# Performance work log

Hardware: AMD Instinct MI355X
Metric: run time of the kernel (lower is better)

Reference implementation:

```python
import jax, jax.numpy as jnp
import numpy as np

B, N = 4, 2048
EXPR, TIME, POSF = 512, 128, 128
H, HD = 8, 64
D = EXPR  # total_features_out_dim == d_model == 512
TOTAL_IN = EXPR + TIME + POSF  # 768
EPS_RMS = 1e-6


def _lin(key, fan_in, fan_out):
    kw, kb = jax.random.split(key)
    lim = 1.0 / np.sqrt(fan_in)
    W = jax.random.uniform(kw, (fan_in, fan_out), minval=-lim, maxval=lim, dtype=jnp.float32)
    b = jax.random.uniform(kb, (fan_out,), minval=-lim, maxval=lim, dtype=jnp.float32)
    return W, b


def setup_inputs() -> dict:
    key = jax.random.key(0)
    ks = jax.random.split(key, 20)
    inp = {}
    inp["expression_features"] = jax.random.normal(ks[0], (B, N, EXPR), dtype=jnp.float32)
    inp["diffusion_time"] = jax.random.normal(ks[1], (B, TIME), dtype=jnp.float32)
    inp["position_features"] = jax.random.normal(ks[2], (B, N, 3), dtype=jnp.float32)
    # position MLP: 4 -> 64 -> POSF
    inp["pos_w1"], inp["pos_b1"] = _lin(ks[3], 4, 64)
    inp["pos_w2"], inp["pos_b2"] = _lin(ks[4], 64, POSF)
    # expression MLP: EXPR -> 64 -> EXPR
    inp["expr_w1"], inp["expr_b1"] = _lin(ks[5], EXPR, 64)
    inp["expr_w2"], inp["expr_b2"] = _lin(ks[6], 64, EXPR)
    # time transform
    inp["yy_w"], inp["yy_b"] = _lin(ks[7], TIME, TIME)
    # concatenated features linear: TOTAL_IN -> D
    inp["cat_w"], inp["cat_b"] = _lin(ks[8], TOTAL_IN, D)
    # attention projections (headwise gating: q_proj outputs D + H)
    inp["q_w"], inp["q_b"] = _lin(ks[9], D, D + H)
    inp["k_w"], inp["k_b"] = _lin(ks[10], D, D)
    inp["v_w"], inp["v_b"] = _lin(ks[11], D, D)
    inp["o_w"], inp["o_b"] = _lin(ks[12], D, D)
    inp["qn_w"] = jnp.ones((HD,), dtype=jnp.float32)
    inp["kn_w"] = jnp.ones((HD,), dtype=jnp.float32)
    # output heads
    inp["hp_w"], inp["hp_b"] = _lin(ks[13], D, 3)
    inp["he_w"], inp["he_b"] = _lin(ks[14], D, EXPR)
    return inp


def _rmsnorm(x, w):
    xf = x.astype(jnp.float32)
    var = jnp.mean(xf * xf, axis=-1, keepdims=True)
    return (w * (xf * jax.lax.rsqrt(var + EPS_RMS))).astype(x.dtype)


def reference(expression_features, diffusion_time, position_features,
              pos_w1, pos_b1, pos_w2, pos_b2,
              expr_w1, expr_b1, expr_w2, expr_b2,
              yy_w, yy_b, cat_w, cat_b,
              q_w, q_b, k_w, k_b, v_w, v_b, o_w, o_b,
              qn_w, kn_w, hp_w, hp_b, he_w, he_b):
    b, n, _ = expression_features.shape
    # expression MLP
    te = jax.nn.relu(expression_features @ expr_w1 + expr_b1) @ expr_w2 + expr_b2
    # position features: direction + norm -> MLP
    nrm = jnp.linalg.norm(position_features, axis=-1, keepdims=True)
    direction = position_features / (nrm + 1e-7)
    pfeat = jnp.concatenate([direction, nrm], axis=-1)  # (B,N,4)
    tp = jax.nn.relu(pfeat @ pos_w1 + pos_b1) @ pos_w2 + pos_b2
    # diffusion time transform (not last layer)
    tdt = diffusion_time @ yy_w + yy_b  # (B,TIME)
    time_exp = jnp.broadcast_to(tdt[:, None, :], (b, n, tdt.shape[-1]))
    cat = jnp.concatenate([te, time_exp, tp], axis=-1)  # (B,N,TOTAL_IN)
    h = cat @ cat_w + cat_b  # (B,N,D)
    # gated multi-head attention
    qfull = h @ q_w + q_b  # (B,N,D+H)
    Q, gate = qfull[..., :D], qfull[..., D:]  # (B,N,D), (B,N,H)
    K = h @ k_w + k_b
    V = h @ v_w + v_b
    Q = Q.reshape(b, n, H, HD).transpose(0, 2, 1, 3)  # (B,H,N,hd)
    K = K.reshape(b, n, H, HD).transpose(0, 2, 1, 3)
    V = V.reshape(b, n, H, HD).transpose(0, 2, 1, 3)
    Q = _rmsnorm(Q, qn_w)
    K = _rmsnorm(K, kn_w)
    scores = jnp.einsum('bhqd,bhkd->bhqk', Q, K) / np.sqrt(HD)
    attn = jax.nn.softmax(scores.astype(jnp.float32), axis=-1).astype(Q.dtype)
    ao = jnp.einsum('bhqk,bhkd->bhqd', attn, V)  # (B,H,N,hd)
    ao = ao.transpose(0, 2, 1, 3)  # (B,N,H,hd)
    ao = ao * jax.nn.sigmoid(gate)[..., None]  # headwise gating
    ao = ao.reshape(b, n, D)
    out = ao @ o_w + o_b  # (B,N,D)
    expr_out = out @ he_w + he_b  # (B,N,EXPR)
    pos_out = out @ hp_w + hp_b   # (B,N,3)
    return expr_out, pos_out, tdt
```

## Files before the change

kernel.cpp:

```cpp
#include <hip/hip_runtime.h>
#include <math.h>

#define SEQ   2048
#define NROWS 8192

typedef unsigned short ushort_t;
typedef __attribute__((ext_vector_type(8))) short bf16x8;
typedef __attribute__((ext_vector_type(4))) float f32x4;

#define U_EXPR   0ull
#define U_A192   4194304ull
#define U_H      5767168ull
#define U_QKV    9961472ull
#define U_KN     26804224ull
#define U_VT     30998528ull
#define U_AO     35192832ull
#define U_W1T    39387136ull
#define U_W2RAW  39419904ull
#define U_CATWT  39452672ull
#define U_QKVWT  39845888ull
#define U_HEWT   40898560ull
#define U_WPRIME 41160704ull
#define U_WOHE   41259008ull
#define U_F32    41521152ull
#define U_ORAW   41537536ull

#define F_TDT    0
#define F_QKVB   512
#define F_BIASH  2056
#define F_BIASEO 4104
#define F_BIASPO 4616
#define F_WHP    4620

#define DOUT_EXPR 0ull
#define DOUT_POS  4194304ull
#define DOUT_TDT  4218880ull

#define LOG2E 1.44269504088896340736f

static __device__ __forceinline__ ushort_t f2bf(float f) {
    union { float f; unsigned int u; } v; v.f = f;
    unsigned int r = (v.u + 0x7fffu + ((v.u >> 16) & 1u)) >> 16;
    return (ushort_t)r;
}
static __device__ __forceinline__ float bf2f(ushort_t u) {
    union { unsigned int u; float f; } v; v.u = ((unsigned int)u) << 16;
    return v.f;
}

static __device__ __forceinline__ void gload16(const void* g, void* l) {
    __builtin_amdgcn_global_load_lds(
        (const __attribute__((address_space(1))) void*)g,
        (__attribute__((address_space(3))) void*)l,
        16, 0, 0);
}

template <int RELU, int OUT_BF16, int HASBIAS, int BBSTRIDE, int KC>
static __device__ void hgemm_body(
    const ushort_t* __restrict__ A, int lda,
    const ushort_t* __restrict__ Wt, int ldw,
    const float* __restrict__ bias,
    void* __restrict__ Cv, int ldc,
    int N, int bx, int by,
    ushort_t* AsB, ushort_t* BsB)
{
    const int tid = threadIdx.x;
    const int lane = tid & 63, w = tid >> 6;
    const int lo = lane & 15, hi = lane >> 4;
    const int wm = w >> 2, wn = w & 3;
    const long m0 = (long)by * 128;
    const int n0 = bx * 128;

    f32x4 acc[4][2];
#pragma unroll
    for (int mt = 0; mt < 4; ++mt)
#pragma unroll
        for (int nt = 0; nt < 2; ++nt) acc[mt][nt] = (f32x4)0.f;

    auto stage = [&](int kt, int buf) {
#pragma unroll
        for (int i = 0; i < 2; ++i) {
            int c = w * 128 + i * 64 + lane;
            int r = c >> 3, ch = c & 7;
            int sch = ch ^ (r & 7);
            gload16(&A[(m0 + r) * (long)lda + kt + sch * 8],
                    &AsB[buf * 8192 + (w * 128 + i * 64) * 8]);
            gload16(&Wt[(long)(n0 + r) * ldw + kt + sch * 8],
                    &BsB[buf * 8192 + (w * 128 + i * 64) * 8]);
        }
    };

    stage(0, 0);
    __syncthreads();

#pragma unroll
    for (int step = 0; step < KC / 64; ++step) {
        const int cur = step & 1;
        if ((step + 1) * 64 < KC) stage((step + 1) * 64, cur ^ 1);

#pragma unroll
        for (int ks = 0; ks < 2; ++ks) {
            bf16x8 af[4], bfr[2];
#pragma unroll
            for (int mt = 0; mt < 4; ++mt) {
                int m = wm * 64 + mt * 16 + lo;
                af[mt] = *(const bf16x8*)&AsB[cur * 8192 + m * 64 +
                                              (((ks * 4 + hi) ^ (lo & 7)) * 8)];
            }
#pragma unroll
            for (int nt = 0; nt < 2; ++nt) {
                int n = wn * 32 + nt * 16 + lo;
                bfr[nt] = *(const bf16x8*)&BsB[cur * 8192 + n * 64 +
                                               (((ks * 4 + hi) ^ (lo & 7)) * 8)];
            }
#pragma unroll
            for (int mt = 0; mt < 4; ++mt)
#pragma unroll
                for (int nt = 0; nt < 2; ++nt)
                    acc[mt][nt] = __builtin_amdgcn_mfma_f32_16x16x32_bf16(
                        af[mt], bfr[nt], acc[mt][nt], 0, 0, 0);
        }
        __syncthreads();
    }

#pragma unroll
    for (int mt = 0; mt < 4; ++mt)
#pragma unroll
        for (int nt = 0; nt < 2; ++nt) {
            int col = n0 + wn * 32 + nt * 16 + lo;
            if (col < N) {
                float bv = 0.f;
                if (HASBIAS)
                    bv = BBSTRIDE ? bias[(int)(m0 >> 11) * BBSTRIDE + col] : bias[col];
#pragma unroll
                for (int r = 0; r < 4; ++r) {
                    long row = m0 + wm * 64 + mt * 16 + hi * 4 + r;
                    float v = acc[mt][nt][r] + bv;
                    if (RELU) v = fmaxf(v, 0.f);
                    if (OUT_BF16) ((ushort_t*)Cv)[row * (long)ldc + col] = f2bf(v);
                    else          ((float*)Cv)[row * (long)ldc + col] = v;
                }
            }
        }
}

template <int RELU, int OUT_BF16, int HASBIAS, int BBSTRIDE, int KC>
__global__ __launch_bounds__(512) void hgemm(
    const ushort_t* __restrict__ A, int lda,
    const ushort_t* __restrict__ Wt, int ldw,
    const float* __restrict__ bias,
    void* __restrict__ Cv, int ldc, int N, int gx)
{
    __shared__ __align__(16) ushort_t ls[32768];
    const int nwg = gridDim.x;
    const int bid = blockIdx.x;
    const int cpx = nwg >> 3;
    const int swz = (bid & 7) * cpx + (bid >> 3);
    hgemm_body<RELU, OUT_BF16, HASBIAS, BBSTRIDE, KC>(
        A, lda, Wt, ldw, bias, Cv, ldc, N,
        swz % gx, swz / gx, ls, ls + 16384);
}

struct WtSeg { const float* src; ushort_t* dst; int K, N, tK, tile0, dstStride, mode; };
struct WtTable { WtSeg s[10]; };

__global__ __launch_bounds__(256) void wt_transpose(
    WtTable tab, const float* __restrict__ qb, const float* __restrict__ kb,
    const float* __restrict__ vb, float* __restrict__ bias_dst,
    const float* __restrict__ dt, const float* __restrict__ yyw,
    const float* __restrict__ yyb, float* __restrict__ tdt_ws,
    float* __restrict__ out_tail)
{
    const int bid = blockIdx.x;
    const int tid = threadIdx.x;
    if (bid == 665) {
        for (int t = tid; t < 512; t += 256) {
            int b = t >> 7, o = t & 127;
            float s = yyb[o];
            for (int k = 0; k < 128; ++k)
                s = fmaf(dt[b * 128 + k], yyw[k * 128 + o], s);
            tdt_ws[t] = s;
            out_tail[t] = s;
        }
        return;
    }
    if (bid >= 658) {
        int t = (bid - 658) * 256 + tid;
        if (t < 520) bias_dst[t] = qb[t];
        else if (t < 1032) bias_dst[t] = kb[t - 520];
        else if (t < 1544) bias_dst[t] = vb[t - 1032];
        return;
    }
    int si = 0;
#pragma unroll
    for (int i = 1; i < 10; ++i)
        if (bid >= tab.s[i].tile0) si = i;
    const WtSeg sg = tab.s[si];
    const int local = bid - sg.tile0;

    if (sg.mode == 1) {
        long base = (long)local * 16384;
#pragma unroll
        for (int i = 0; i < 8; ++i) {
            long p = base + i * 2048 + tid * 8;
            float4 a = *(const float4*)&sg.src[p];
            float4 b = *(const float4*)&sg.src[p + 4];
            bf16x8 o;
            o[0] = (short)f2bf(a.x); o[1] = (short)f2bf(a.y);
            o[2] = (short)f2bf(a.z); o[3] = (short)f2bf(a.w);
            o[4] = (short)f2bf(b.x); o[5] = (short)f2bf(b.y);
            o[6] = (short)f2bf(b.z); o[7] = (short)f2bf(b.w);
            *(bf16x8*)&sg.dst[p] = o;
        }
        return;
    }

    __shared__ float t[64][65];
    const int k0 = (local % sg.tK) * 64;
    const int n0 = (local / sg.tK) * 64;
#pragma unroll
    for (int i = 0; i < 16; ++i) {
        int e = tid + i * 256;
        int r = e >> 6, c = e & 63;
        float v = 0.f;
        if (k0 + r < sg.K && n0 + c < sg.N)
            v = sg.src[(long)(k0 + r) * sg.N + n0 + c];
        t[r][c] = v;
    }
    __syncthreads();
#pragma unroll
    for (int i = 0; i < 16; ++i) {
        int e = tid + i * 256;
        int rn = e >> 6, ck = e & 63;
        if (n0 + rn < sg.N && k0 + ck < sg.K)
            sg.dst[(long)(n0 + rn) * sg.dstStride + k0 + ck] = f2bf(t[ck][rn]);
    }
}

__global__ __launch_bounds__(512) void prep2mlp_kernel(
    const ushort_t* __restrict__ catwt, const ushort_t* __restrict__ hewt,
    const ushort_t* __restrict__ w2raw, const ushort_t* __restrict__ o_raw,
    ushort_t* __restrict__ wprime, ushort_t* __restrict__ wohe,
    const float* __restrict__ expr_b2, const float* __restrict__ tdt,
    const float* __restrict__ cat_b, const float* __restrict__ o_b,
    const float* __restrict__ he_b, const float* __restrict__ o_w,
    const float* __restrict__ hp_w, const float* __restrict__ hp_b,
    float* __restrict__ bias_h, float* __restrict__ bias_eo,
    float* __restrict__ whp, float* __restrict__ bias_po,
    const ushort_t* __restrict__ expr_bf, const ushort_t* __restrict__ w1t,
    const float* __restrict__ expr_b1,
    const float* __restrict__ pos,
    const float* __restrict__ w1, const float* __restrict__ b1,
    const float* __restrict__ w2, const float* __restrict__ b2,
    ushort_t* __restrict__ a192)
{
    __shared__ __align__(16) ushort_t ls[32768];
    const int bid = blockIdx.x;
    const int tid = threadIdx.x;

    if (bid < 4) {
        hgemm_body<0, 1, 0, 0, 512>(catwt, 768, w2raw, 512, nullptr, wprime, 192,
                                    64, 0, bid, ls, ls + 16384);
        return;
    }
    if (bid < 20) {
        int local = bid - 4;
        hgemm_body<0, 1, 0, 0, 512>(hewt, 512, o_raw, 512, nullptr, wohe, 512,
                                    512, local & 3, local >> 2, ls, ls + 16384);
        return;
    }
    if (bid < 533) {
        const int wid = (bid - 20) * 8 + (tid >> 6);
        const int lane = tid & 63;
        float s = 0.f;
        if (wid < 2048) {
            int b = wid >> 9, n = wid & 511;
            bf16x8 wv = *(const bf16x8*)&catwt[(long)n * 768 + lane * 8];
            float4 e0 = *(const float4*)&expr_b2[lane * 8];
            float4 e1 = *(const float4*)&expr_b2[lane * 8 + 4];
            s = bf2f((ushort_t)wv[0]) * e0.x + bf2f((ushort_t)wv[1]) * e0.y +
                bf2f((ushort_t)wv[2]) * e0.z + bf2f((ushort_t)wv[3]) * e0.w +
                bf2f((ushort_t)wv[4]) * e1.x + bf2f((ushort_t)wv[5]) * e1.y +
                bf2f((ushort_t)wv[6]) * e1.z + bf2f((ushort_t)wv[7]) * e1.w;
            float2 tt = *(const float2*)&tdt[b * 128 + lane * 2];
            s += bf2f(catwt[(long)n * 768 + 512 + lane * 2]) * tt.x;
            s += bf2f(catwt[(long)n * 768 + 513 + lane * 2]) * tt.y;
#pragma unroll
            for (int o = 32; o >= 1; o >>= 1) s += __shfl_xor(s, o);
            if (lane == 0) bias_h[b * 512 + n] = s + cat_b[n];
        } else if (wid < 2560) {
            int n = wid - 2048;
            bf16x8 wv = *(const bf16x8*)&hewt[(long)n * 512 + lane * 8];
            float4 e0 = *(const float4*)&o_b[lane * 8];
            float4 e1 = *(const float4*)&o_b[lane * 8 + 4];
            s = bf2f((ushort_t)wv[0]) * e0.x + bf2f((ushort_t)wv[1]) * e0.y +
                bf2f((ushort_t)wv[2]) * e0.z + bf2f((ushort_t)wv[3]) * e0.w +
                bf2f((ushort_t)wv[4]) * e1.x + bf2f((ushort_t)wv[5]) * e1.y +
                bf2f((ushort_t)wv[6]) * e1.z + bf2f((ushort_t)wv[7]) * e1.w;
#pragma unroll
            for (int o = 32; o >= 1; o >>= 1) s += __shfl_xor(s, o);
            if (lane == 0) bias_eo[n] = s + he_b[n];
        } else if (wid < 4096) {
            int t = wid - 2560;
            int c = t >> 9, k = t & 511;
#pragma unroll
            for (int i = 0; i < 8; ++i) {
                int j = i * 64 + lane;
                s = fmaf(o_w[(long)k * 512 + j], hp_w[j * 3 + c], s);
            }
#pragma unroll
            for (int o = 32; o >= 1; o >>= 1) s += __shfl_xor(s, o);
            if (lane == 0) whp[k * 3 + c] = s;
        } else if (wid < 4099) {
            int c = wid - 4096;
#pragma unroll
            for (int i = 0; i < 8; ++i) {
                int j = i * 64 + lane;
                s = fmaf(o_b[j], hp_w[j * 3 + c], s);
            }
#pragma unroll
            for (int o = 32; o >= 1; o >>= 1) s += __shfl_xor(s, o);
            if (lane == 0) bias_po[c] = s + hp_b[c];
        }
        return;
    }
    if (bid < 597) {
        hgemm_body<1, 1, 1, 0, 512>(expr_bf, 512, w1t, 512, expr_b1, a192, 192,
                                    64, 0, bid - 533, ls, ls + 16384);
        return;
    }

    float* w1s = (float*)ls;
    float* b1s = w1s + 256;
    float* b2s = b1s + 64;
    float* w2t = b2s + 128;
    if (tid < 256) w1s[tid] = w1[tid];
    if (tid >= 256 && tid < 320) b1s[tid - 256] = b1[tid - 256];
    if (tid >= 320 && tid < 448) b2s[tid - 320] = b2[tid - 320];
    for (int i = tid; i < 8192; i += 512) {
        int k = i >> 7, o = i & 127;
        w2t[o * 72 + k] = w2[i];
    }
    __syncthreads();

    const long r = (long)(bid - 597) * 64 + (tid >> 3);
    const int chunk = tid & 7;
    float px = pos[r * 3 + 0], py = pos[r * 3 + 1], pz = pos[r * 3 + 2];
    float nrm = sqrtf(px * px + py * py + pz * pz);
    float inv = 1.f / (nrm + 1e-7f);
    float pf0 = px * inv, pf1 = py * inv, pf2 = pz * inv, pf3 = nrm;

    float h1[64];
#pragma unroll
    for (int o = 0; o < 64; ++o) {
        float a = b1s[o];
        a = fmaf(pf0, w1s[o], a);
        a = fmaf(pf1, w1s[64 + o], a);
        a = fmaf(pf2, w1s[128 + o], a);
        a = fmaf(pf3, w1s[192 + o], a);
        h1[o] = fmaxf(a, 0.f);
    }
    ushort_t* dst = &a192[r * 192 + 64];
#pragma unroll
    for (int j = 0; j < 16; ++j) {
        int o = chunk + 8 * j;
        float s = b2s[o];
#pragma unroll
        for (int i4 = 0; i4 < 16; ++i4) {
            float4 wv = *(const float4*)&w2t[o * 72 + i4 * 4];
            s = fmaf(h1[i4 * 4 + 0], wv.x, s);
            s = fmaf(h1[i4 * 4 + 1], wv.y, s);
            s = fmaf(h1[i4 * 4 + 2], wv.z, s);
            s = fmaf(h1[i4 * 4 + 3], wv.w, s);
        }
        dst[o] = f2bf(s);
    }
}

__global__ __launch_bounds__(256) void qkvpost_kernel(
    const ushort_t* __restrict__ qkv, const float* __restrict__ knw,
    ushort_t* __restrict__ kn, ushort_t* __restrict__ Vt)
{
    __shared__ ushort_t t[64][72];
    __shared__ float knw_s[64];
    const int bh = blockIdx.x, b = bh >> 3, h = bh & 7;
    const int n0 = blockIdx.y * 64;
    const int tid = threadIdx.x;
    if (tid < 64) knw_s[tid] = knw[tid];
#pragma unroll
    for (int i = 0; i < 2; ++i) {
        int c = tid + i * 256;
        int r = c >> 3, ch = c & 7;
        *(bf16x8*)&t[r][ch * 8] =
            *(const bf16x8*)&qkv[(long)(b * SEQ + n0 + r) * 1544 + 1032 + h * 64 + ch * 8];
    }
    __syncthreads();
#pragma unroll
    for (int i = 0; i < 2; ++i) {
        int c = tid + i * 256;
        int r = c >> 3, ch = c & 7;
        bf16x8 kv = *(const bf16x8*)&qkv[(long)(b * SEQ + n0 + r) * 1544 + 520 + h * 64 + ch * 8];
        float x[8], ss = 0.f;
#pragma unroll
        for (int j = 0; j < 8; ++j) { x[j] = bf2f((ushort_t)kv[j]); ss = fmaf(x[j], x[j], ss); }
        ss += __shfl_xor(ss, 1);
        ss += __shfl_xor(ss, 2);
        ss += __shfl_xor(ss, 4);
        float invr = rsqrtf(ss * (1.f / 64.f) + 1e-6f);
        bf16x8 o;
#pragma unroll
        for (int j = 0; j < 8; ++j) o[j] = (short)f2bf(x[j] * knw_s[ch * 8 + j] * invr);
        *(bf16x8*)&kn[(long)(b * SEQ + n0 + r) * 512 + h * 64 + ch * 8] = o;
    }
    const int d = tid >> 2;
#pragma unroll
    for (int i = 0; i < 2; ++i) {
        int cc = (tid & 3) * 2 + i;
        bf16x8 pk;
#pragma unroll
        for (int j = 0; j < 8; ++j) pk[j] = (short)t[cc * 8 + j][d];
        *(bf16x8*)&Vt[((long)(bh * 64 + d)) * SEQ + n0 + cc * 8] = pk;
    }
}

__global__ __launch_bounds__(256) void flash_attn_mfma(
    const ushort_t* __restrict__ QKV, const ushort_t* __restrict__ Kn,
    const ushort_t* __restrict__ Vt, const float* __restrict__ qnw,
    ushort_t* __restrict__ AO)
{
    __shared__ __align__(16) ushort_t Ks[2][64 * 64];
    __shared__ __align__(16) ushort_t Vs[2][64 * 64];
    __shared__ __align__(16) ushort_t Ps[4][32 * 64];

    const int tid = threadIdx.x;
    const int lane = tid & 63;
    const int w = tid >> 6;
    const int lo = lane & 15, hi = lane >> 4;
    const int bh = blockIdx.x, b = bh >> 3, h = bh & 7;
    const int qb = blockIdx.y * 128 + w * 32;

    bf16x8 qfrag[2][2];
    {
        float qw[2][8];
#pragma unroll
        for (int ks = 0; ks < 2; ++ks)
#pragma unroll
            for (int j = 0; j < 8; ++j)
                qw[ks][j] = qnw[ks * 32 + hi * 8 + j];
#pragma unroll
        for (int jt = 0; jt < 2; ++jt) {
            float qx[2][8], ss = 0.f;
#pragma unroll
            for (int ks = 0; ks < 2; ++ks) {
                bf16x8 q = *(const bf16x8*)&QKV[(long)(b * SEQ + qb + jt * 16 + lo) * 1544 +
                                                h * 64 + ks * 32 + hi * 8];
#pragma unroll
                for (int j = 0; j < 8; ++j) {
                    qx[ks][j] = bf2f((ushort_t)q[j]);
                    ss = fmaf(qx[ks][j], qx[ks][j], ss);
                }
            }
            ss += __shfl_xor(ss, 16);
            ss += __shfl_xor(ss, 32);
            float invr = rsqrtf(ss * (1.f / 64.f) + 1e-6f) * (0.125f * LOG2E);
#pragma unroll
            for (int ks = 0; ks < 2; ++ks) {
                bf16x8 f;
#pragma unroll
                for (int j = 0; j < 8; ++j)
                    f[j] = (short)f2bf(qx[ks][j] * qw[ks][j] * invr);
                qfrag[jt][ks] = f;
            }
        }
    }

    f32x4 accO[2][4];
#pragma unroll
    for (int mt = 0; mt < 2; ++mt)
#pragma unroll
        for (int nt = 0; nt < 4; ++nt) accO[mt][nt] = (f32x4)0.f;
    float l_part[2] = {0.f, 0.f};

    const int sr0 = tid >> 3, sc0 = tid & 7;
    const int sr1 = (tid + 256) >> 3, sc1 = tid & 7;
    const int wo0 = sr0 * 64 + ((sc0 ^ (sr0 & 7)) * 8);
    const int wo1 = sr1 * 64 + ((sc1 ^ (sr1 & 7)) * 8);

    bf16x8 kreg0, kreg1, vreg0, vreg1;
    kreg0 = *(const bf16x8*)&Kn[(b * SEQ + sr0) * 512 + h * 64 + sc0 * 8];
    vreg0 = *(const bf16x8*)&Vt[((long)(bh * 64 + sr0)) * SEQ + sc0 * 8];
    kreg1 = *(const bf16x8*)&Kn[(b * SEQ + sr1) * 512 + h * 64 + sc1 * 8];
    vreg1 = *(const bf16x8*)&Vt[((long)(bh * 64 + sr1)) * SEQ + sc1 * 8];
    *(bf16x8*)&Ks[0][wo0] = kreg0;
    *(bf16x8*)&Vs[0][wo0] = vreg0;
    *(bf16x8*)&Ks[0][wo1] = kreg1;
    *(bf16x8*)&Vs[0][wo1] = vreg1;
    kreg0 = *(const bf16x8*)&Kn[(b * SEQ + 64 + sr0) * 512 + h * 64 + sc0 * 8];
    vreg0 = *(const bf16x8*)&Vt[((long)(bh * 64 + sr0)) * SEQ + 64 + sc0 * 8];
    kreg1 = *(const bf16x8*)&Kn[(b * SEQ + 64 + sr1) * 512 + h * 64 + sc1 * 8];
    vreg1 = *(const bf16x8*)&Vt[((long)(bh * 64 + sr1)) * SEQ + 64 + sc1 * 8];
    __syncthreads();

    auto step = [&](int kt, int cur, int nxt) {
        if (kt + 1 < 32) {
            *(bf16x8*)&Ks[nxt][wo0] = kreg0;
            *(bf16x8*)&Vs[nxt][wo0] = vreg0;
            *(bf16x8*)&Ks[nxt][wo1] = kreg1;
            *(bf16x8*)&Vs[nxt][wo1] = vreg1;
        }
        if (kt + 2 < 32) {
            int nk = (kt + 2) * 64;
            kreg0 = *(const bf16x8*)&Kn[(b * SEQ + nk + sr0) * 512 + h * 64 + sc0 * 8];
            vreg0 = *(const bf16x8*)&Vt[((long)(bh * 64 + sr0)) * SEQ + nk + sc0 * 8];
            kreg1 = *(const bf16x8*)&Kn[(b * SEQ + nk + sr1) * 512 + h * 64 + sc1 * 8];
            vreg1 = *(const bf16x8*)&Vt[((long)(bh * 64 + sr1)) * SEQ + nk + sc1 * 8];
        }

        f32x4 accS[4][2];
#pragma unroll
        for (int it = 0; it < 4; ++it)
#pragma unroll
            for (int jt = 0; jt < 2; ++jt) accS[it][jt] = (f32x4)0.f;

#pragma unroll
        for (int it = 0; it < 4; ++it) {
            bf16x8 kf[2];
#pragma unroll
            for (int ks = 0; ks < 2; ++ks)
                kf[ks] = *(const bf16x8*)&Ks[cur][(it * 16 + lo) * 64 +
                                                 (((ks * 4 + hi) ^ (lo & 7)) * 8)];
#pragma unroll
            for (int jt = 0; jt < 2; ++jt)
#pragma unroll
                for (int ks = 0; ks < 2; ++ks)
                    accS[it][jt] = __builtin_amdgcn_mfma_f32_16x16x32_bf16(
                        kf[ks], qfrag[jt][ks], accS[it][jt], 0, 0, 0);
        }

#pragma unroll
        for (int it = 0; it < 4; ++it)
#pragma unroll
            for (int jt = 0; jt < 2; ++jt) {
                float p0, p1, p2, p3;
                asm("v_exp_f32 %0, %1" : "=v"(p0) : "v"(accS[it][jt][0]));
                asm("v_exp_f32 %0, %1" : "=v"(p1) : "v"(accS[it][jt][1]));
                asm("v_exp_f32 %0, %1" : "=v"(p2) : "v"(accS[it][jt][2]));
                asm("v_exp_f32 %0, %1" : "=v"(p3) : "v"(accS[it][jt][3]));
                l_part[jt] += (p0 + p1) + (p2 + p3);
                unsigned w0, w1;
                asm("v_cvt_pk_bf16_f32 %0, %1, %2" : "=v"(w0) : "v"(p0), "v"(p1));
                asm("v_cvt_pk_bf16_f32 %0, %1, %2" : "=v"(w1) : "v"(p2), "v"(p3));
                int q = jt * 16 + lo;
                int cch = it * 2 + (hi >> 1);
                int off = q * 64 + ((cch ^ (q & 7)) * 8) + (hi & 1) * 4;
                uint2 t; t.x = w0; t.y = w1;
                *(uint2*)&Ps[w][off] = t;
            }

#pragma unroll
        for (int kk = 0; kk < 2; ++kk) {
            bf16x8 pf[2];
#pragma unroll
            for (int mt = 0; mt < 2; ++mt)
                pf[mt] = *(const bf16x8*)&Ps[w][(mt * 16 + lo) * 64 +
                                               (((kk * 4 + hi) ^ (lo & 7)) * 8)];
#pragma unroll
            for (int nt = 0; nt < 4; ++nt) {
                bf16x8 vf = *(const bf16x8*)&Vs[cur][(nt * 16 + lo) * 64 +
                                                    (((kk * 4 + hi) ^ (lo & 7)) * 8)];
#pragma unroll
                for (int mt = 0; mt < 2; ++mt)
                    accO[mt][nt] = __builtin_amdgcn_mfma_f32_16x16x32_bf16(
                        pf[mt], vf, accO[mt][nt], 0, 0, 0);
            }
        }
        __syncthreads();
    };

    for (int kt = 0; kt < 32; kt += 2) {
        step(kt, 0, 1);
        step(kt + 1, 1, 0);
    }

#pragma unroll
    for (int jt = 0; jt < 2; ++jt) {
        l_part[jt] += __shfl_xor(l_part[jt], 16);
        l_part[jt] += __shfl_xor(l_part[jt], 32);
    }

#pragma unroll
    for (int mt = 0; mt < 2; ++mt)
#pragma unroll
        for (int r = 0; r < 4; ++r) {
            float lq = __shfl(l_part[mt], hi * 4 + r);
            int grow = b * SEQ + qb + mt * 16 + hi * 4 + r;
            float g = bf2f(QKV[(long)grow * 1544 + 512 + h]);
            g = 1.f / (1.f + __expf(-g));
            float sc = g / lq;
#pragma unroll
            for (int nt = 0; nt < 4; ++nt)
                AO[(long)grow * 512 + h * 64 + nt * 16 + lo] = f2bf(accO[mt][nt][r] * sc);
        }
}

__global__ __launch_bounds__(512) void out_kernel(
    const ushort_t* __restrict__ ao, const ushort_t* __restrict__ wohe,
    const float* __restrict__ bias_eo, float* __restrict__ eo,
    const float* __restrict__ whp, const float* __restrict__ bpo,
    float* __restrict__ po)
{
    __shared__ __align__(16) ushort_t ls[32768];
    const int bid = blockIdx.x;
    const int tid = threadIdx.x;

    if (bid < 256) {
        hgemm_body<0, 0, 1, 0, 512>(ao, 512, wohe, 512, bias_eo, eo, 512,
                                    512, bid & 3, bid >> 2, ls, ls + 16384);
        return;
    }

    const int lane = tid & 63;
    const long row = (long)(bid - 256) * 8 + (tid >> 6);
    float p0 = 0.f, p1 = 0.f, p2 = 0.f;
#pragma unroll
    for (int it = 0; it < 8; ++it) {
        int k = it * 64 + lane;
        float x = bf2f(ao[row * 512 + k]);
        p0 = fmaf(x, whp[k * 3 + 0], p0);
        p1 = fmaf(x, whp[k * 3 + 1], p1);
        p2 = fmaf(x, whp[k * 3 + 2], p2);
    }
#pragma unroll
    for (int o = 32; o >= 1; o >>= 1) {
        p0 += __shfl_xor(p0, o);
        p1 += __shfl_xor(p1, o);
        p2 += __shfl_xor(p2, o);
    }
    if (lane == 0) {
        po[row * 3 + 0] = p0 + bpo[0];
        po[row * 3 + 1] = p1 + bpo[1];
        po[row * 3 + 2] = p2 + bpo[2];
    }
}

extern "C" void kernel_launch(void* const* d_in, const int* in_sizes, int n_in,
                              void* d_out, int out_size, void* d_ws, size_t ws_size,
                              hipStream_t stream)
{
    const float* expr    = (const float*)d_in[0];
    const float* dtime   = (const float*)d_in[1];
    const float* posf    = (const float*)d_in[2];
    const float* pos_w1  = (const float*)d_in[3];
    const float* pos_b1  = (const float*)d_in[4];
    const float* pos_w2  = (const float*)d_in[5];
    const float* pos_b2  = (const float*)d_in[6];
    const float* expr_w1 = (const float*)d_in[7];
    const float* expr_b1 = (const float*)d_in[8];
    const float* expr_w2 = (const float*)d_in[9];
    const float* expr_b2 = (const float*)d_in[10];
    const float* yy_w    = (const float*)d_in[11];
    const float* yy_b    = (const float*)d_in[12];
    const float* cat_w   = (const float*)d_in[13];
    const float* cat_b   = (const float*)d_in[14];
    const float* q_w     = (const float*)d_in[15];
    const float* q_b     = (const float*)d_in[16];
    const float* k_w     = (const float*)d_in[17];
    const float* k_b     = (const float*)d_in[18];
    const float* v_w     = (const float*)d_in[19];
    const float* v_b     = (const float*)d_in[20];
    const float* o_w     = (const float*)d_in[21];
    const float* o_b     = (const float*)d_in[22];
    const float* qn_w    = (const float*)d_in[23];
    const float* kn_w    = (const float*)d_in[24];
    const float* hp_w    = (const float*)d_in[25];
    const float* hp_b    = (const float*)d_in[26];
    const float* he_w    = (const float*)d_in[27];
    const float* he_b    = (const float*)d_in[28];
    (void)in_sizes; (void)n_in; (void)out_size; (void)ws_size;

    ushort_t* wsb     = (ushort_t*)d_ws;
    ushort_t* expr_bf = wsb + U_EXPR;
    ushort_t* a192    = wsb + U_A192;
    ushort_t* h_bf    = wsb + U_H;
    ushort_t* qkv_bf  = wsb + U_QKV;
    ushort_t* kn_bf   = wsb + U_KN;
    ushort_t* vt_bf   = wsb + U_VT;
    ushort_t* ao_bf   = wsb + U_AO;
    ushort_t* w1t     = wsb + U_W1T;
    ushort_t* w2raw   = wsb + U_W2RAW;
    ushort_t* cat_wt  = wsb + U_CATWT;
    ushort_t* qkv_wt  = wsb + U_QKVWT;
    ushort_t* he_wt   = wsb + U_HEWT;
    ushort_t* wprime  = wsb + U_WPRIME;
    ushort_t* wohe    = wsb + U_WOHE;
    ushort_t* o_raw   = wsb + U_ORAW;
    float* f32r       = (float*)(wsb + U_F32);
    float* tdt        = f32r + F_TDT;
    float* qkv_bias   = f32r + F_QKVB;
    float* bias_h     = f32r + F_BIASH;
    float* bias_eo    = f32r + F_BIASEO;
    float* bias_po    = f32r + F_BIASPO;
    float* whp        = f32r + F_WHP;
    float* dout       = (float*)d_out;

    const dim3 blk(256);
    const dim3 blk512(512);

    WtTable tab;
    tab.s[0] = { expr_w1,          w1t,             512,  64,  8,   0, 512, 0 };
    tab.s[1] = { cat_w,            cat_wt,          768, 512, 12,   8, 768, 0 };
    tab.s[2] = { q_w,              qkv_wt,          512, 520,  8, 104, 512, 0 };
    tab.s[3] = { k_w,              qkv_wt + 520*512,512, 512,  8, 176, 512, 0 };
    tab.s[4] = { v_w,              qkv_wt +1032*512,512, 512,  8, 240, 512, 0 };
    tab.s[5] = { he_w,             he_wt,           512, 512,  8, 304, 512, 0 };
    tab.s[6] = { cat_w + 640*512,  wprime + 64,     128, 512,  2, 368, 192, 0 };
    tab.s[7] = { expr_w2,          w2raw,             0,   0,  0, 384,   0, 1 };
    tab.s[8] = { o_w,              o_raw,             0,   0,  0, 386,   0, 1 };
    tab.s[9] = { expr,             expr_bf,           0,   0,  0, 402,   0, 1 };
    wt_transpose<<<dim3(666), blk, 0, stream>>>(tab, q_b, k_b, v_b, qkv_bias,
                                                dtime, yy_w, yy_b, tdt,
                                                dout + DOUT_TDT);

    prep2mlp_kernel<<<dim3(725), blk512, 0, stream>>>(
        cat_wt, he_wt, w2raw, o_raw, wprime, wohe,
        expr_b2, tdt, cat_b, o_b, he_b, o_w, hp_w, hp_b,
        bias_h, bias_eo, whp, bias_po,
        expr_bf, w1t, expr_b1, posf, pos_w1, pos_b1, pos_w2, pos_b2, a192);

    hgemm<0, 1, 1, 512, 192><<<dim3(256), blk512, 0, stream>>>(
        a192, 192, wprime, 192, bias_h, h_bf, 512, 512, 4);
    hgemm<0, 1, 1, 0, 512><<<dim3(832), blk512, 0, stream>>>(
        h_bf, 512, qkv_wt, 512, qkv_bias, qkv_bf, 1544, 1544, 13);
    qkvpost_kernel<<<dim3(32, 32), blk, 0, stream>>>(qkv_bf, kn_w, kn_bf, vt_bf);
    flash_attn_mfma<<<dim3(32, 16), blk, 0, stream>>>(qkv_bf, kn_bf, vt_bf, qn_w, ao_bf);
    out_kernel<<<dim3(1280), blk512, 0, stream>>>(
        ao_bf, wohe, bias_eo, dout + DOUT_EXPR, whp, bias_po, dout + DOUT_POS);
}
```

Measured before the change: 124.3 us.

## Double query rows per wave in flash attention to reuse K/V tiles

Each wave now handles 64 query rows instead of 32, so each block covers 256 queries and the grid drops from 512 to 256 blocks. Every K/V tile loaded into shared memory then feeds twice as many MFMAs, halving global K/V traffic and LDS staging per query. The S computation is split into two halves to limit register pressure, and launch_bounds(256,1) gives the compiler a larger register budget. The cost is fewer blocks (256 on a 256-CU part, one wave set per CU), lower occupancy and less latency hiding, plus a larger P buffer in shared memory.

```diff
diff --git a/kernel.cpp b/kernel.cpp
--- a/kernel.cpp
+++ b/kernel.cpp
@@ -423,23 +423,23 @@
     }
 }
 
-__global__ __launch_bounds__(256) void flash_attn_mfma(
+__global__ __launch_bounds__(256, 1) void flash_attn_mfma(
     const ushort_t* __restrict__ QKV, const ushort_t* __restrict__ Kn,
     const ushort_t* __restrict__ Vt, const float* __restrict__ qnw,
     ushort_t* __restrict__ AO)
 {
     __shared__ __align__(16) ushort_t Ks[2][64 * 64];
     __shared__ __align__(16) ushort_t Vs[2][64 * 64];
-    __shared__ __align__(16) ushort_t Ps[4][32 * 64];
+    __shared__ __align__(16) ushort_t Ps[4][64 * 64];
 
     const int tid = threadIdx.x;
     const int lane = tid & 63;
     const int w = tid >> 6;
     const int lo = lane & 15, hi = lane >> 4;
     const int bh = blockIdx.x, b = bh >> 3, h = bh & 7;
-    const int qb = blockIdx.y * 128 + w * 32;
-
-    bf16x8 qfrag[2][2];
+    const int qb = blockIdx.y * 256 + w * 64;
+
+    bf16x8 qfrag[4][2];
     {
         float qw[2][8];
 #pragma unroll
@@ -448,7 +448,7 @@
             for (int j = 0; j < 8; ++j)
                 qw[ks][j] = qnw[ks * 32 + hi * 8 + j];
 #pragma unroll
-        for (int jt = 0; jt < 2; ++jt) {
+        for (int jt = 0; jt < 4; ++jt) {
             float qx[2][8], ss = 0.f;
 #pragma unroll
             for (int ks = 0; ks < 2; ++ks) {
@@ -474,12 +474,12 @@
         }
     }
 
-    f32x4 accO[2][4];
-#pragma unroll
-    for (int mt = 0; mt < 2; ++mt)
+    f32x4 accO[4][4];
+#pragma unroll
+    for (int mt = 0; mt < 4; ++mt)
 #pragma unroll
         for (int nt = 0; nt < 4; ++nt) accO[mt][nt] = (f32x4)0.f;
-    float l_part[2] = {0.f, 0.f};
+    float l_part[4] = {0.f, 0.f, 0.f, 0.f};
 
     const int sr0 = tid >> 3, sc0 = tid & 7;
     const int sr1 = (tid + 256) >> 3, sc1 = tid & 7;
@@ -516,52 +516,58 @@
             vreg1 = *(const bf16x8*)&Vt[((long)(bh * 64 + sr1)) * SEQ + nk + sc1 * 8];
         }
 
-        f32x4 accS[4][2];
-#pragma unroll
-        for (int it = 0; it < 4; ++it)
-#pragma unroll
-            for (int jt = 0; jt < 2; ++jt) accS[it][jt] = (f32x4)0.f;
-
-#pragma unroll
-        for (int it = 0; it < 4; ++it) {
-            bf16x8 kf[2];
-#pragma unroll
-            for (int ks = 0; ks < 2; ++ks)
-                kf[ks] = *(const bf16x8*)&Ks[cur][(it * 16 + lo) * 64 +
-                                                 (((ks * 4 + hi) ^ (lo & 7)) * 8)];
-#pragma unroll
-            for (int jt = 0; jt < 2; ++jt)
+#pragma unroll
+        for (int ith = 0; ith < 2; ++ith) {
+            f32x4 accS[2][4];
+#pragma unroll
+            for (int it2 = 0; it2 < 2; ++it2)
+#pragma unroll
+                for (int jt = 0; jt < 4; ++jt) accS[it2][jt] = (f32x4)0.f;
+
+#pragma unroll
+            for (int it2 = 0; it2 < 2; ++it2) {
+                const int it = ith * 2 + it2;
+                bf16x8 kf[2];
 #pragma unroll
                 for (int ks = 0; ks < 2; ++ks)
-                    accS[it][jt] = __builtin_amdgcn_mfma_f32_16x16x32_bf16(
-                        kf[ks], qfrag[jt][ks], accS[it][jt], 0, 0, 0);
-        }
-
-#pragma unroll
-        for (int it = 0; it < 4; ++it)
-#pragma unroll
-            for (int jt = 0; jt < 2; ++jt) {
-                float p0, p1, p2, p3;
-                asm("v_exp_f32 %0, %1" : "=v"(p0) : "v"(accS[it][jt][0]));
-                asm("v_exp_f32 %0, %1" : "=v"(p1) : "v"(accS[it][jt][1]));
-                asm("v_exp_f32 %0, %1" : "=v"(p2) : "v"(accS[it][jt][2]));
-                asm("v_exp_f32 %0, %1" : "=v"(p3) : "v"(accS[it][jt][3]));
-                l_part[jt] += (p0 + p1) + (p2 + p3);
-                unsigned w0, w1;
-                asm("v_cvt_pk_bf16_f32 %0, %1, %2" : "=v"(w0) : "v"(p0), "v"(p1));
-                asm("v_cvt_pk_bf16_f32 %0, %1, %2" : "=v"(w1) : "v"(p2), "v"(p3));
-                int q = jt * 16 + lo;
-                int cch = it * 2 + (hi >> 1);
-                int off = q * 64 + ((cch ^ (q & 7)) * 8) + (hi & 1) * 4;
-                uint2 t; t.x = w0; t.y = w1;
-                *(uint2*)&Ps[w][off] = t;
-            }
+                    kf[ks] = *(const bf16x8*)&Ks[cur][(it * 16 + lo) * 64 +
+                                                     (((ks * 4 + hi) ^ (lo & 7)) * 8)];
+#pragma unroll
+                for (int jt = 0; jt < 4; ++jt)
+#pragma unroll
+                    for (int ks = 0; ks < 2; ++ks)
+                        accS[it2][jt] = __builtin_amdgcn_mfma_f32_16x16x32_bf16(
+                            kf[ks], qfrag[jt][ks], accS[it2][jt], 0, 0, 0);
+            }
+
+#pragma unroll
+            for (int it2 = 0; it2 < 2; ++it2) {
+                const int it = ith * 2 + it2;
+#pragma unroll
+                for (int jt = 0; jt < 4; ++jt) {
+                    float p0, p1, p2, p3;
+                    asm("v_exp_f32 %0, %1" : "=v"(p0) : "v"(accS[it2][jt][0]));
+                    asm("v_exp_f32 %0, %1" : "=v"(p1) : "v"(accS[it2][jt][1]));
+                    asm("v_exp_f32 %0, %1" : "=v"(p2) : "v"(accS[it2][jt][2]));
+                    asm("v_exp_f32 %0, %1" : "=v"(p3) : "v"(accS[it2][jt][3]));
+                    l_part[jt] += (p0 + p1) + (p2 + p3);
+                    unsigned w0, w1;
+                    asm("v_cvt_pk_bf16_f32 %0, %1, %2" : "=v"(w0) : "v"(p0), "v"(p1));
+                    asm("v_cvt_pk_bf16_f32 %0, %1, %2" : "=v"(w1) : "v"(p2), "v"(p3));
+                    int q = jt * 16 + lo;
+                    int cch = it * 2 + (hi >> 1);
+                    int off = q * 64 + ((cch ^ (q & 7)) * 8) + (hi & 1) * 4;
+                    uint2 t; t.x = w0; t.y = w1;
+                    *(uint2*)&Ps[w][off] = t;
+                }
+            }
+        }
 
 #pragma unroll
         for (int kk = 0; kk < 2; ++kk) {
-            bf16x8 pf[2];
-#pragma unroll
-            for (int mt = 0; mt < 2; ++mt)
+            bf16x8 pf[4];
+#pragma unroll
+            for (int mt = 0; mt < 4; ++mt)
                 pf[mt] = *(const bf16x8*)&Ps[w][(mt * 16 + lo) * 64 +
                                                (((kk * 4 + hi) ^ (lo & 7)) * 8)];
 #pragma unroll
@@ -569,7 +575,7 @@
                 bf16x8 vf = *(const bf16x8*)&Vs[cur][(nt * 16 + lo) * 64 +
                                                     (((kk * 4 + hi) ^ (lo & 7)) * 8)];
 #pragma unroll
-                for (int mt = 0; mt < 2; ++mt)
+                for (int mt = 0; mt < 4; ++mt)
                     accO[mt][nt] = __builtin_amdgcn_mfma_f32_16x16x32_bf16(
                         pf[mt], vf, accO[mt][nt], 0, 0, 0);
             }
@@ -583,13 +589,13 @@
     }
 
 #pragma unroll
-    for (int jt = 0; jt < 2; ++jt) {
+    for (int jt = 0; jt < 4; ++jt) {
         l_part[jt] += __shfl_xor(l_part[jt], 16);
         l_part[jt] += __shfl_xor(l_part[jt], 32);
     }
 
 #pragma unroll
-    for (int mt = 0; mt < 2; ++mt)
+    for (int mt = 0; mt < 4; ++mt)
 #pragma unroll
         for (int r = 0; r < 4; ++r) {
             float lq = __shfl(l_part[mt], hi * 4 + r);
@@ -732,7 +738,7 @@
     hgemm<0, 1, 1, 0, 512><<<dim3(832), blk512, 0, stream>>>(
         h_bf, 512, qkv_wt, 512, qkv_bias, qkv_bf, 1544, 1544, 13);
     qkvpost_kernel<<<dim3(32, 32), blk, 0, stream>>>(qkv_bf, kn_w, kn_bf, vt_bf);
-    flash_attn_mfma<<<dim3(32, 16), blk, 0, stream>>>(qkv_bf, kn_bf, vt_bf, qn_w, ao_bf);
+    flash_attn_mfma<<<dim3(32, 8), blk, 0, stream>>>(qkv_bf, kn_bf, vt_bf, qn_w, ao_bf);
     out_kernel<<<dim3(1280), blk512, 0, stream>>>(
         ao_bf, wohe, bias_eo, dout + DOUT_EXPR, whp, bias_po, dout + DOUT_POS);
 }
```

Measured after the change: 128.4 us. +3.3%, slower.
